# Optimization experiments

Hardware: AMD Instinct MI355X
Metric: run time of the kernel (lower is better)

## Reference

```python
import jax, jax.numpy as jnp
import numpy as np

N_NODES = 50000
N_EDGES = 800000
IN_DIM = 256
OUT_DIM = 64


def setup_inputs() -> dict:
    key = jax.random.key(0)
    k1, k2, k3, k4, k5 = jax.random.split(key, 5)
    input = jax.random.normal(k1, (N_NODES, IN_DIM), dtype=jnp.float32)
    # Xavier-uniform-like weight, zero bias (as in the torch module)
    limit = float(np.sqrt(6.0 / (IN_DIM + OUT_DIM)))
    weight = jax.random.uniform(k2, (IN_DIM, OUT_DIM), dtype=jnp.float32, minval=-limit, maxval=limit)
    bias = jnp.zeros((OUT_DIM,), dtype=jnp.float32)
    # COO representation of the sparse normalized adjacency
    edge_val = jax.random.uniform(k3, (N_EDGES,), dtype=jnp.float32)
    edge_src = jax.random.randint(k4, (N_EDGES,), 0, N_NODES, dtype=jnp.int64)
    edge_dst = jax.random.randint(k5, (N_EDGES,), 0, N_NODES, dtype=jnp.int64)
    return {"input": input, "weight": weight, "bias": bias,
            "edge_val": edge_val, "edge_src": edge_src, "edge_dst": edge_dst}


def reference(input, weight, bias, edge_val, edge_src, edge_dst):
    # support = input @ W  -> [N, out_dim]
    support = jnp.dot(input, weight)
    # spmm(adj, support): gather source rows, scale by edge weight, scatter-add into dst
    msgs = support[edge_src] * edge_val[:, None]        # [E, out_dim]
    output = jax.ops.segment_sum(msgs, edge_dst, num_segments=N_NODES)
    return output + bias
```

## Files before the change

kernel.cpp:

```cpp
#include <hip/hip_runtime.h>

#define N_NODES 50000
#define N_EDGES 800000
#define IN_DIM  256
#define OUT_DIM 64
#define NB      196

#define WS_SUPPORT 0
#define WS_COUNTS  12800000
#define WS_OFFSETS 13000064
#define WS_CURSOR  13200128
#define WS_BSUM    13400128
#define WS_BOFF    13400960
#define WS_RECS    13401792

__global__ __launch_bounds__(512) void gcn_gemm(const float* __restrict__ input,
                                                const float* __restrict__ W,
                                                float* __restrict__ support)
{
    __shared__ float Xs[64][64];
    const int tid  = threadIdx.x;
    const int lane = tid & 63;
    const int w    = __builtin_amdgcn_readfirstlane(tid >> 6);
    const int c0   = w * 8;
    const int r0   = blockIdx.x * 64;

    float acc[8] = {0.f,0.f,0.f,0.f,0.f,0.f,0.f,0.f};
    const float* Wb = W + c0;

    for (int kc = 0; kc < 4; ++kc) {
        #pragma unroll
        for (int it = 0; it < 2; ++it) {
            const int F  = it * 512 + tid;
            const int r  = F >> 4;
            const int k4 = (F & 15) * 4;
            int rr = r0 + r; if (rr > N_NODES - 1) rr = N_NODES - 1;
            const float4 xv = *(const float4*)(input + (size_t)rr * IN_DIM + kc * 64 + k4);
            Xs[r][(k4 + 0 + r) & 63] = xv.x;
            Xs[r][(k4 + 1 + r) & 63] = xv.y;
            Xs[r][(k4 + 2 + r) & 63] = xv.z;
            Xs[r][(k4 + 3 + r) & 63] = xv.w;
        }
        __syncthreads();
        const float* Wk = Wb + (size_t)(kc * 64) * OUT_DIM;
        #pragma unroll 8
        for (int k6 = 0; k6 < 64; ++k6) {
            const float x = Xs[lane][(k6 + lane) & 63];
            const float* wrow = Wk + (size_t)k6 * OUT_DIM;
            #pragma unroll
            for (int j = 0; j < 8; ++j)
                acc[j] += x * wrow[j];
        }
        __syncthreads();
    }

    const int row = r0 + lane;
    if (row < N_NODES) {
        float* op = support + (size_t)row * OUT_DIM + c0;
        *(float4*)(op)     = make_float4(acc[0], acc[1], acc[2], acc[3]);
        *(float4*)(op + 4) = make_float4(acc[4], acc[5], acc[6], acc[7]);
    }
}

__global__ __launch_bounds__(256) void gcn_hist(const int* __restrict__ dst,
                                                int* __restrict__ counts)
{
    const int e = blockIdx.x * 256 + threadIdx.x;
    if (e < N_EDGES) atomicAdd(&counts[dst[e]], 1);
}

__global__ __launch_bounds__(256) void gcn_scanA(const int* __restrict__ counts,
                                                 int* __restrict__ bsum)
{
    __shared__ int wsum[4];
    const int tid = threadIdx.x, lane = tid & 63, wid = tid >> 6;
    const int i = blockIdx.x * 256 + tid;
    int v = (i < N_NODES) ? counts[i] : 0;
    #pragma unroll
    for (int d = 32; d > 0; d >>= 1) v += __shfl_down(v, d);
    if (lane == 0) wsum[wid] = v;
    __syncthreads();
    if (tid == 0) bsum[blockIdx.x] = wsum[0] + wsum[1] + wsum[2] + wsum[3];
}

__global__ __launch_bounds__(256) void gcn_scanB(const int* __restrict__ bsum,
                                                 int* __restrict__ boff)
{
    __shared__ int wsum[4];
    const int tid = threadIdx.x, lane = tid & 63, wid = tid >> 6;
    const int orig = (tid < NB) ? bsum[tid] : 0;
    int v = orig;
    #pragma unroll
    for (int d = 1; d < 64; d <<= 1) {
        const int u = __shfl_up(v, d);
        if (lane >= d) v += u;
    }
    if (lane == 63) wsum[wid] = v;
    __syncthreads();
    int pre = 0;
    for (int ww = 0; ww < wid; ++ww) pre += wsum[ww];
    if (tid < NB) boff[tid] = pre + v - orig;
}

__global__ __launch_bounds__(256) void gcn_scanC(const int* __restrict__ counts,
                                                 const int* __restrict__ boff,
                                                 int* __restrict__ offsets,
                                                 int* __restrict__ cursor)
{
    __shared__ int wsum[4];
    const int tid = threadIdx.x, lane = tid & 63, wid = tid >> 6;
    const int i = blockIdx.x * 256 + tid;
    const int orig = (i < N_NODES) ? counts[i] : 0;
    int v = orig;
    #pragma unroll
    for (int d = 1; d < 64; d <<= 1) {
        const int u = __shfl_up(v, d);
        if (lane >= d) v += u;
    }
    if (lane == 63) wsum[wid] = v;
    __syncthreads();
    int pre = boff[blockIdx.x];
    for (int ww = 0; ww < wid; ++ww) pre += wsum[ww];
    const int excl = pre + v - orig;
    if (i < N_NODES) { offsets[i] = excl; cursor[i] = excl; }
    if (i == N_NODES - 1) offsets[N_NODES] = excl + orig;
}

__global__ __launch_bounds__(256) void gcn_build(const int*   __restrict__ src,
                                                 const int*   __restrict__ dst,
                                                 const float* __restrict__ val,
                                                 int*  __restrict__ cursor,
                                                 int2* __restrict__ recs)
{
    const int e = blockIdx.x * 256 + threadIdx.x;
    if (e < N_EDGES) {
        const int d   = dst[e];
        const int pos = atomicAdd(&cursor[d], 1);
        recs[pos] = make_int2(src[e], __float_as_int(val[e]));
    }
}

__global__ __launch_bounds__(256) void gcn_gather(const float* __restrict__ support,
                                                  const int2*  __restrict__ recs,
                                                  const int*   __restrict__ offsets,
                                                  const float* __restrict__ bias,
                                                  float* __restrict__ out)
{
    const int lane = threadIdx.x & 63;
    const int n = __builtin_amdgcn_readfirstlane(
                      (int)((blockIdx.x * 256 + threadIdx.x) >> 6));
    if (n >= N_NODES) return;

    const float b   = bias[lane];
    const int   beg = offsets[n];
    const int   end = offsets[n + 1];
    float acc = 0.f;
    int i = beg;

    if (end - beg >= 8) {
        int2 ra = recs[i],   rb = recs[i+1], rc = recs[i+2], rd = recs[i+3];
        float sa = support[(size_t)ra.x * OUT_DIM + lane];
        float sb = support[(size_t)rb.x * OUT_DIM + lane];
        float sc = support[(size_t)rc.x * OUT_DIM + lane];
        float sd = support[(size_t)rd.x * OUT_DIM + lane];
        for (; i + 8 <= end; i += 4) {
            const int2 na = recs[i+4], nb = recs[i+5], nc = recs[i+6], nd = recs[i+7];
            const float ta = support[(size_t)na.x * OUT_DIM + lane];
            const float tb = support[(size_t)nb.x * OUT_DIM + lane];
            const float tc = support[(size_t)nc.x * OUT_DIM + lane];
            const float td = support[(size_t)nd.x * OUT_DIM + lane];
            acc += __int_as_float(ra.y) * sa;
            acc += __int_as_float(rb.y) * sb;
            acc += __int_as_float(rc.y) * sc;
            acc += __int_as_float(rd.y) * sd;
            ra = na; sa = ta;  rb = nb; sb = tb;
            rc = nc; sc = tc;  rd = nd; sd = td;
        }
        acc += __int_as_float(ra.y) * sa + __int_as_float(rb.y) * sb
             + __int_as_float(rc.y) * sc + __int_as_float(rd.y) * sd;
        i += 4;
    }
    for (; i < end; ++i) {
        const int2 r = recs[i];
        acc += __int_as_float(r.y) * support[(size_t)r.x * OUT_DIM + lane];
    }
    out[(size_t)n * OUT_DIM + lane] = acc + b;
}

extern "C" void kernel_launch(void* const* d_in, const int* in_sizes, int n_in,
                              void* d_out, int out_size, void* d_ws, size_t ws_size,
                              hipStream_t stream)
{
    const float* input  = (const float*)d_in[0];
    const float* weight = (const float*)d_in[1];
    const float* bias   = (const float*)d_in[2];
    const float* eval_  = (const float*)d_in[3];
    const int*   esrc   = (const int*)d_in[4];
    const int*   edst   = (const int*)d_in[5];
    float*       out    = (float*)d_out;

    char* ws = (char*)d_ws;
    float* support = (float*)(ws + WS_SUPPORT);
    int*   counts  = (int*)(ws + WS_COUNTS);
    int*   offsets = (int*)(ws + WS_OFFSETS);
    int*   cursor  = (int*)(ws + WS_CURSOR);
    int*   bsum    = (int*)(ws + WS_BSUM);
    int*   boff    = (int*)(ws + WS_BOFF);
    int2*  recs    = (int2*)(ws + WS_RECS);

    hipMemsetAsync(counts, 0, N_NODES * sizeof(int), stream);

    gcn_gemm<<<(N_NODES + 63) / 64, 512, 0, stream>>>(input, weight, support);

    gcn_hist <<<(N_EDGES + 255) / 256, 256, 0, stream>>>(edst, counts);
    gcn_scanA<<<NB, 256, 0, stream>>>(counts, bsum);
    gcn_scanB<<<1, 256, 0, stream>>>(bsum, boff);
    gcn_scanC<<<NB, 256, 0, stream>>>(counts, boff, offsets, cursor);
    gcn_build<<<(N_EDGES + 255) / 256, 256, 0, stream>>>(esrc, edst, eval_, cursor, recs);

    gcn_gather<<<(N_NODES * 64) / 256, 256, 0, stream>>>(support, recs, offsets, bias, out);
}
```

Baseline: 250.1 us.

## Drop LDS staging in GEMM and bucket CSR build by destination range

The GEMM now has each wave load its own row's 64-element K chunk straight into registers as float4s instead of staging it through shared memory with barriers. Blocks shrink to 256 threads and there are more of them. The build kernel has 8 blocks share each 4096-edge chunk, and each block keeps only the edges whose destination falls into its eighth of the node range. This is meant to localise atomic and record-write traffic to a narrower address window, at the cost of reading each dst index eight times. The register-held x arrays raise register pressure, and the input reads become strided per lane (one row per lane).

```diff
diff --git a/kernel.cpp b/kernel.cpp
--- a/kernel.cpp
+++ b/kernel.cpp
@@ -5,6 +5,8 @@
 #define IN_DIM  256
 #define OUT_DIM 64
 #define NB      196
+#define CHUNK   4096
+#define NCHUNK  196
 
 #define WS_SUPPORT 0
 #define WS_COUNTS  12800000
@@ -14,47 +16,41 @@
 #define WS_BOFF    13400960
 #define WS_RECS    13401792
 
-__global__ __launch_bounds__(512) void gcn_gemm(const float* __restrict__ input,
+__global__ __launch_bounds__(256) void gcn_gemm(const float* __restrict__ input,
                                                 const float* __restrict__ W,
                                                 float* __restrict__ support)
 {
-    __shared__ float Xs[64][64];
     const int tid  = threadIdx.x;
     const int lane = tid & 63;
-    const int w    = __builtin_amdgcn_readfirstlane(tid >> 6);
-    const int c0   = w * 8;
-    const int r0   = blockIdx.x * 64;
+    const int gw   = __builtin_amdgcn_readfirstlane(
+                         (int)((blockIdx.x * 256 + tid) >> 6));
+    const int rg   = gw >> 3;
+    const int c0   = (gw & 7) * 8;
+    if (rg >= (N_NODES + 63) / 64) return;
+
+    int row = rg * 64 + lane;
+    const int rowc = row < N_NODES ? row : N_NODES - 1;
+    const float* xp = input + (size_t)rowc * IN_DIM;
+    const float* Wc = W + c0;
 
     float acc[8] = {0.f,0.f,0.f,0.f,0.f,0.f,0.f,0.f};
-    const float* Wb = W + c0;
 
     for (int kc = 0; kc < 4; ++kc) {
+        float4 xv[16];
         #pragma unroll
-        for (int it = 0; it < 2; ++it) {
-            const int F  = it * 512 + tid;
-            const int r  = F >> 4;
-            const int k4 = (F & 15) * 4;
-            int rr = r0 + r; if (rr > N_NODES - 1) rr = N_NODES - 1;
-            const float4 xv = *(const float4*)(input + (size_t)rr * IN_DIM + kc * 64 + k4);
-            Xs[r][(k4 + 0 + r) & 63] = xv.x;
-            Xs[r][(k4 + 1 + r) & 63] = xv.y;
-            Xs[r][(k4 + 2 + r) & 63] = xv.z;
-            Xs[r][(k4 + 3 + r) & 63] = xv.w;
-        }
-        __syncthreads();
-        const float* Wk = Wb + (size_t)(kc * 64) * OUT_DIM;
-        #pragma unroll 8
+        for (int f = 0; f < 16; ++f)
+            xv[f] = *(const float4*)(xp + kc * 64 + f * 4);
+        const float* Wk = Wc + (size_t)(kc * 64) * OUT_DIM;
+        #pragma unroll
         for (int k6 = 0; k6 < 64; ++k6) {
-            const float x = Xs[lane][(k6 + lane) & 63];
+            const float x = ((const float*)xv)[k6];
             const float* wrow = Wk + (size_t)k6 * OUT_DIM;
             #pragma unroll
             for (int j = 0; j < 8; ++j)
                 acc[j] += x * wrow[j];
         }
-        __syncthreads();
-    }
-
-    const int row = r0 + lane;
+    }
+
     if (row < N_NODES) {
         float* op = support + (size_t)row * OUT_DIM + c0;
         *(float4*)(op)     = make_float4(acc[0], acc[1], acc[2], acc[3]);
@@ -132,11 +128,18 @@
                                                  int*  __restrict__ cursor,
                                                  int2* __restrict__ recs)
 {
-    const int e = blockIdx.x * 256 + threadIdx.x;
-    if (e < N_EDGES) {
-        const int d   = dst[e];
-        const int pos = atomicAdd(&cursor[d], 1);
-        recs[pos] = make_int2(src[e], __float_as_int(val[e]));
+    const int s  = blockIdx.x & 7;
+    const int e0 = (blockIdx.x >> 3) * CHUNK;
+    #pragma unroll 4
+    for (int t = threadIdx.x; t < CHUNK; t += 256) {
+        const int e = e0 + t;
+        if (e < N_EDGES) {
+            const int d = dst[e];
+            if (((d * 21475) >> 27) == s) {
+                const int pos = atomicAdd(&cursor[d], 1);
+                recs[pos] = make_int2(src[e], __float_as_int(val[e]));
+            }
+        }
     }
 }
 
@@ -210,13 +213,13 @@
 
     hipMemsetAsync(counts, 0, N_NODES * sizeof(int), stream);
 
-    gcn_gemm<<<(N_NODES + 63) / 64, 512, 0, stream>>>(input, weight, support);
+    gcn_gemm<<<1564, 256, 0, stream>>>(input, weight, support);
 
     gcn_hist <<<(N_EDGES + 255) / 256, 256, 0, stream>>>(edst, counts);
     gcn_scanA<<<NB, 256, 0, stream>>>(counts, bsum);
     gcn_scanB<<<1, 256, 0, stream>>>(bsum, boff);
     gcn_scanC<<<NB, 256, 0, stream>>>(counts, boff, offsets, cursor);
-    gcn_build<<<(N_EDGES + 255) / 256, 256, 0, stream>>>(esrc, edst, eval_, cursor, recs);
+    gcn_build<<<NCHUNK * 8, 256, 0, stream>>>(esrc, edst, eval_, cursor, recs);
 
     gcn_gather<<<(N_NODES * 64) / 256, 256, 0, stream>>>(support, recs, offsets, bias, out);
 }
```

New measurement: 258.6 us. 1.03x slower.
